# Kernel optimization log

Hardware: AMD Instinct MI355X
Metric: run time of the kernel (lower is better)

## Reference

```python
import jax, jax.numpy as jnp
import numpy as np

N_NODES = 100000
N_EDGES = 800000
IN_DIM = 128
NUM_HEADS = 8
HEAD_DIM = 16  # out_dim // num_heads = 128 // 8


def setup_inputs() -> dict:
    key = jax.random.key(0)
    ks = jax.random.split(key, 10)
    scale = 1.0 / np.sqrt(IN_DIM)
    return {
        "x": jax.random.normal(ks[0], (N_NODES, IN_DIM), dtype=jnp.float32),
        "edge_index": jax.random.randint(ks[1], (2, N_EDGES), 0, N_NODES, dtype=jnp.int64),
        "virt_h": jax.random.normal(ks[2], (1, IN_DIM), dtype=jnp.float32),
        "virt_edge_index": jax.random.randint(ks[3], (2, 1), 0, 1, dtype=jnp.int64),
        "Wq": jax.random.normal(ks[4], (IN_DIM, NUM_HEADS * HEAD_DIM), dtype=jnp.float32) * scale,
        "bq": jnp.zeros((NUM_HEADS * HEAD_DIM,), dtype=jnp.float32),
        "Wk": jax.random.normal(ks[5], (IN_DIM, NUM_HEADS * HEAD_DIM), dtype=jnp.float32) * scale,
        "bk": jnp.zeros((NUM_HEADS * HEAD_DIM,), dtype=jnp.float32),
        "Wv": jax.random.normal(ks[6], (IN_DIM, NUM_HEADS * HEAD_DIM), dtype=jnp.float32) * scale,
        "bv": jnp.zeros((NUM_HEADS * HEAD_DIM,), dtype=jnp.float32),
    }


def reference(x, edge_index, virt_h, virt_edge_index, Wq, bq, Wk, bk, Wv, bv):
    # use_virt_nodes=False: virt_h / virt_edge_index are unused dummies.
    n = x.shape[0]
    H, D = NUM_HEADS, HEAD_DIM
    Q = (x @ Wq + bq).reshape(n, H, D)
    K = (x @ Wk + bk).reshape(n, H, D)
    V = (x @ Wv + bv).reshape(n, H, D)

    src = edge_index[0]
    dst = edge_index[1]

    # edge-wise gather QK dot -> clamp -> exp; score: [E, H, 1]
    dot = jnp.sum(K[src] * Q[dst], axis=-1, keepdims=True) / np.sqrt(D).astype(np.float32)
    score = jnp.exp(jnp.clip(dot, -5.0, 5.0))

    msg = V[src] * score  # [E, H, D]
    wV = jax.ops.segment_sum(msg, dst, num_segments=n)     # [N, H, D]
    Z = jax.ops.segment_sum(score, dst, num_segments=n)    # [N, H, 1]

    h_out = (wV / (Z + 1e-6)).reshape(n, H * D)
    return h_out
```

## Files before the change

### kernel.cpp

```cpp
#include <hip/hip_runtime.h>

#define IN_DIM   128
#define NH       8
#define HD       16
#define OUTD     128
#define QKVD     384
#define SH       7
#define NSORTB   128
#define GRID     1024

typedef unsigned short ushort_t;
typedef unsigned int   uint_t;
typedef __bf16 bf16x8 __attribute__((ext_vector_type(8)));
typedef float  f32x4  __attribute__((ext_vector_type(4)));

__device__ __forceinline__ float bf2f(ushort_t u) {
    return __uint_as_float(((uint_t)u) << 16);
}
__device__ __forceinline__ ushort_t f2bf(float f) {
    uint_t u = __float_as_uint(f);
    u += 0x7FFFu + ((u >> 16) & 1u);
    return (ushort_t)(u >> 16);
}

__global__ __launch_bounds__(256) void prep_w(
    const float* __restrict__ Wq, const float* __restrict__ Wk,
    const float* __restrict__ Wv, ushort_t* __restrict__ Wt)
{
    __shared__ float ld[32][33];
    int mat  = blockIdx.x >> 4;
    int tile = blockIdx.x & 15;
    int k0 = (tile >> 2) * 32, c0 = (tile & 3) * 32;
    const float* W = (mat == 0) ? Wq : (mat == 1) ? Wk : Wv;
    int t = threadIdx.x;
    {
        int k = t >> 3, c4 = (t & 7) * 4;
        float4 f = *(const float4*)&W[(size_t)(k0 + k) * 128 + c0 + c4];
        ld[k][c4 + 0] = f.x; ld[k][c4 + 1] = f.y;
        ld[k][c4 + 2] = f.z; ld[k][c4 + 3] = f.w;
    }
    __syncthreads();
    {
        int c = t >> 3, kg = (t & 7) * 4;
        union { ushort_t h[4]; uint2 u; } o;
        o.h[0] = f2bf(ld[kg + 0][c]); o.h[1] = f2bf(ld[kg + 1][c]);
        o.h[2] = f2bf(ld[kg + 2][c]); o.h[3] = f2bf(ld[kg + 3][c]);
        *(uint2*)&Wt[((size_t)(mat * 128 + c0 + c)) * 128 + k0 + kg] = o.u;
    }
}

__global__ __launch_bounds__(384, 3) void fat_gemm_sort(
    const float* __restrict__ x, const ushort_t* __restrict__ Wt,
    const float* __restrict__ bq, const float* __restrict__ bk,
    const float* __restrict__ bv, ushort_t* __restrict__ qkv,
    const int* __restrict__ ei, int* __restrict__ aux,
    uint_t* __restrict__ regions,
    int N, int E, int ntiles, int NBC, int CH)
{
    __shared__ __align__(16) char smem[33192];

    if (blockIdx.x < NSORTB) {
        uint_t* recs = (uint_t*)smem;
        int* hist    = (int*)(smem + 25000);
        int* scn     = (int*)(smem + 29096);
        const int tid = threadIdx.x;
        const int blk = blockIdx.x;
        const int e0g = blk * CH;
        const int e1g = min(E, e0g + CH);
        const int m   = e1g - e0g;

        for (int i = tid; i < 1024; i += 384) hist[i] = 0;
        __syncthreads();
        for (int e = e0g + tid; e < e1g; e += 384)
            atomicAdd(&hist[ei[E + e] >> SH], 1);
        __syncthreads();
        if (tid < 64) {
            int base16 = tid * 16;
            int loc[16]; int s = 0;
#pragma unroll
            for (int i = 0; i < 16; i++) { loc[i] = s; s += hist[base16 + i]; }
            int incl = s;
            for (int off = 1; off < 64; off <<= 1) {
                int t = __shfl_up(incl, off);
                if (tid >= off) incl += t;
            }
            int cexcl = incl - s;
#pragma unroll
            for (int i = 0; i < 16; i++) scn[base16 + i] = cexcl + loc[i];
        }
        __syncthreads();
        for (int b = tid; b < NBC; b += 384) aux[b * NSORTB + blk] = scn[b];
        if (tid == 0) aux[NBC * NSORTB + blk] = m;
        __syncthreads();
        for (int e = e0g + tid; e < e1g; e += 384) {
            int d = ei[E + e];
            int src = ei[e];
            int slot = atomicAdd(&scn[d >> SH], 1);
            recs[slot] = (uint_t)src | ((uint_t)(d & 127) << 20);
        }
        __syncthreads();
        for (int s = tid; s < m; s += 384)
            regions[(size_t)blk * CH + s] = recs[s];
        return;
    }

    ushort_t* sh = (ushort_t*)smem;

    const int tid  = threadIdx.x;
    const int w    = tid >> 6;
    const int quad = (tid >> 4) & 3;
    const int l15  = tid & 15;
    const int colg = w << 6;

    bf16x8 bfr[4][4];
#pragma unroll
    for (int kt = 0; kt < 4; kt++)
#pragma unroll
        for (int cs = 0; cs < 4; cs++) {
            int col = colg + cs * 16 + l15;
            bfr[kt][cs] = *(const bf16x8*)&Wt[(size_t)col * 128 + kt * 32 + quad * 8];
        }

    const int mat = w >> 1;
    const float* Bp = (mat == 0) ? bq : (mat == 1) ? bk : bv;
    float bias[4];
#pragma unroll
    for (int cs = 0; cs < 4; cs++)
        bias[cs] = Bp[((w & 1) << 6) + cs * 16 + l15];

    const int gstride = (int)gridDim.x - NSORTB;
    for (int tile = (int)blockIdx.x - NSORTB; tile < ntiles; tile += gstride) {
        const int row0 = tile * 64;
        __syncthreads();

        for (int ch = tid; ch < 1024; ch += 384) {
            int row = ch >> 4;
            int kc  = ch & 15;
            int grow = row0 + row; if (grow > N - 1) grow = N - 1;
            const float* xp = x + (size_t)grow * IN_DIM + kc * 8;
            float4 f0 = *(const float4*)xp;
            float4 f1 = *(const float4*)(xp + 4);
            union { ushort_t h[8]; uint4 u; } tt;
            tt.h[0] = f2bf(f0.x); tt.h[1] = f2bf(f0.y);
            tt.h[2] = f2bf(f0.z); tt.h[3] = f2bf(f0.w);
            tt.h[4] = f2bf(f1.x); tt.h[5] = f2bf(f1.y);
            tt.h[6] = f2bf(f1.z); tt.h[7] = f2bf(f1.w);
            *(uint4*)&sh[(kc * 65 + row) * 8] = tt.u;
        }
        __syncthreads();

        f32x4 acc[4][4];
#pragma unroll
        for (int r = 0; r < 4; r++)
#pragma unroll
            for (int cs = 0; cs < 4; cs++) acc[r][cs] = (f32x4){0.f, 0.f, 0.f, 0.f};

#pragma unroll
        for (int kt = 0; kt < 4; kt++) {
            int kc = kt * 4 + quad;
            bf16x8 af[4];
#pragma unroll
            for (int r = 0; r < 4; r++)
                af[r] = *(const bf16x8*)&sh[(kc * 65 + r * 16 + l15) * 8];
#pragma unroll
            for (int r = 0; r < 4; r++)
#pragma unroll
                for (int cs = 0; cs < 4; cs++)
                    acc[r][cs] = __builtin_amdgcn_mfma_f32_16x16x32_bf16(
                        af[r], bfr[kt][cs], acc[r][cs], 0, 0, 0);
        }

#define EPS 392
#pragma unroll
        for (int qq = 0; qq < 4; qq++) {
            __syncthreads();
            int lrow = quad << 2;
#pragma unroll
            for (int cs = 0; cs < 4; cs++) {
                int col = (w << 6) + cs * 16 + l15;
#pragma unroll
                for (int reg = 0; reg < 4; reg++)
                    sh[(lrow + reg) * EPS + col] = f2bf(acc[qq][cs][reg] + bias[cs]);
            }
            __syncthreads();
#pragma unroll
            for (int i = 0; i < 2; i++) {
                int c = tid + i * 384;
                int row = c / 48;
                int col = (c % 48) * 8;
                int grow = row0 + qq * 16 + row;
                if (grow < N) {
                    uint4 val = *(const uint4*)&sh[row * EPS + col];
                    *(uint4*)&qkv[(size_t)grow * QKVD + col] = val;
                }
            }
        }
#undef EPS
    }
}

__global__ __launch_bounds__(256) void efine(
    const uint_t* __restrict__ regions, const int* __restrict__ aux,
    int* __restrict__ P, int* __restrict__ sorted_src,
    int N, int NBC, int CH)
{
    __shared__ int rl[128], ro[128], doff[128];
    __shared__ int cnt[128], scn2[128];
    __shared__ uint_t stage[4096];
    __shared__ int    sst[4096];
    __shared__ int s_part[2];
    const int tid = threadIdx.x;
    const int b   = blockIdx.x;

    if (tid < 128) {
        int r0 = aux[b * NSORTB + tid];
        int r1 = aux[(b + 1) * NSORTB + tid];
        ro[tid] = r0;
        rl[tid] = r1 - r0;
        doff[tid] = r1 - r0;
        int bsum = r0;
#pragma unroll
        for (int off = 1; off < 64; off <<= 1)
            bsum += __shfl_xor(bsum, off);
        if ((tid & 63) == 0) s_part[tid >> 6] = bsum;
    }
    __syncthreads();
    for (int off = 1; off < 128; off <<= 1) {
        int v = (tid >= off && tid < 128) ? doff[tid - off] : 0;
        __syncthreads();
        if (tid < 128) doff[tid] += v;
        __syncthreads();
    }
    const int m = doff[127];
    const int base = s_part[0] + s_part[1];

    {
        int r = tid >> 1, k = tid & 1;
        int dst0 = doff[r] - rl[r];
        int src0 = ro[r];
        int len  = rl[r];
        for (int i = k; i < len; i += 2)
            stage[dst0 + i] = regions[(size_t)r * CH + src0 + i];
    }
    __syncthreads();

    if (tid < 128) cnt[tid] = 0;
    __syncthreads();
    for (int i = tid; i < m; i += 256)
        atomicAdd(&cnt[stage[i] >> 20], 1);
    __syncthreads();
    if (tid < 128) scn2[tid] = cnt[tid];
    __syncthreads();
    for (int off = 1; off < 128; off <<= 1) {
        int v = (tid >= off && tid < 128) ? scn2[tid - off] : 0;
        __syncthreads();
        if (tid < 128) scn2[tid] += v;
        __syncthreads();
    }
    if (tid < 128) {
        int excl = scn2[tid] - cnt[tid];
        int n = b * 128 + tid;
        if (n < N) P[n] = base + excl;
        cnt[tid] = excl;
    }
    __syncthreads();
    for (int i = tid; i < m; i += 256) {
        uint_t r = stage[i];
        int pos = atomicAdd(&cnt[r >> 20], 1);
        sst[pos] = (int)(r & 0xFFFFFu);
    }
    __syncthreads();
    for (int i = tid; i < m; i += 256)
        sorted_src[base + i] = sst[i];
}

__global__ __launch_bounds__(256) void segment_attn(
    const ushort_t* __restrict__ qkv,
    const int* __restrict__ P, const int* __restrict__ sorted_src,
    float* __restrict__ out, int N, int E)
{
    int n = (blockIdx.x * 256 + threadIdx.x) >> 4;
    int g = threadIdx.x & 15;
    if (n >= N) return;
    int start = P[n];
    int end   = (n + 1 < N) ? P[n + 1] : E;
    int deg   = end - start;

    const uint_t* qrow = (const uint_t*)(qkv + (size_t)n * QKVD);
    uint4 qu = *(const uint4*)(qrow + g * 4);
    float q0 = bf2f((ushort_t)(qu.x & 0xFFFF)), q1 = bf2f((ushort_t)(qu.x >> 16));
    float q2 = bf2f((ushort_t)(qu.y & 0xFFFF)), q3 = bf2f((ushort_t)(qu.y >> 16));
    float q4 = bf2f((ushort_t)(qu.z & 0xFFFF)), q5 = bf2f((ushort_t)(qu.z >> 16));
    float q6 = bf2f((ushort_t)(qu.w & 0xFFFF)), q7 = bf2f((ushort_t)(qu.w >> 16));

    float a0 = 0.f, a1 = 0.f, a2 = 0.f, a3 = 0.f;
    float a4 = 0.f, a5 = 0.f, a6 = 0.f, a7 = 0.f, z = 0.f;

    int myidx = (g < deg) ? sorted_src[start + g] : 0;
    int wbase = (threadIdx.x & 63) & 48;

#define PROC(ku, vu)                                                       \
    {                                                                      \
        float p = bf2f((ushort_t)((ku).x & 0xFFFF)) * q0                   \
                + bf2f((ushort_t)((ku).x >> 16))    * q1                   \
                + bf2f((ushort_t)((ku).y & 0xFFFF)) * q2                   \
                + bf2f((ushort_t)((ku).y >> 16))    * q3                   \
                + bf2f((ushort_t)((ku).z & 0xFFFF)) * q4                   \
                + bf2f((ushort_t)((ku).z >> 16))    * q5                   \
                + bf2f((ushort_t)((ku).w & 0xFFFF)) * q6                   \
                + bf2f((ushort_t)((ku).w >> 16))    * q7;                  \
        p += __shfl_xor(p, 1);                                             \
        p = fminf(fmaxf(p * 0.25f, -5.f), 5.f);                            \
        float s = __expf(p);                                               \
        a0 += bf2f((ushort_t)((vu).x & 0xFFFF)) * s;                       \
        a1 += bf2f((ushort_t)((vu).x >> 16))    * s;                       \
        a2 += bf2f((ushort_t)((vu).y & 0xFFFF)) * s;                       \
        a3 += bf2f((ushort_t)((vu).y >> 16))    * s;                       \
        a4 += bf2f((ushort_t)((vu).z & 0xFFFF)) * s;                       \
        a5 += bf2f((ushort_t)((vu).z >> 16))    * s;                       \
        a6 += bf2f((ushort_t)((vu).w & 0xFFFF)) * s;                       \
        a7 += bf2f((ushort_t)((vu).w >> 16))    * s;                       \
        z += s;                                                            \
    }

    int cnt = (deg < 16) ? deg : 16;
    int t = 0;
    for (; t + 4 <= cnt; t += 4) {
        int s0 = __shfl(myidx, wbase + t);
        int s1 = __shfl(myidx, wbase + t + 1);
        int s2 = __shfl(myidx, wbase + t + 2);
        int s3 = __shfl(myidx, wbase + t + 3);
        const uint_t* kv0 = (const uint_t*)(qkv + (size_t)s0 * QKVD + 128);
        const uint_t* kv1 = (const uint_t*)(qkv + (size_t)s1 * QKVD + 128);
        const uint_t* kv2 = (const uint_t*)(qkv + (size_t)s2 * QKVD + 128);
        const uint_t* kv3 = (const uint_t*)(qkv + (size_t)s3 * QKVD + 128);
        uint4 ku0 = *(const uint4*)(kv0 + g * 4);
        uint4 ku1 = *(const uint4*)(kv1 + g * 4);
        uint4 ku2 = *(const uint4*)(kv2 + g * 4);
        uint4 ku3 = *(const uint4*)(kv3 + g * 4);
        uint4 vu0 = *(const uint4*)(kv0 + 64 + g * 4);
        uint4 vu1 = *(const uint4*)(kv1 + 64 + g * 4);
        uint4 vu2 = *(const uint4*)(kv2 + 64 + g * 4);
        uint4 vu3 = *(const uint4*)(kv3 + 64 + g * 4);
        PROC(ku0, vu0); PROC(ku1, vu1); PROC(ku2, vu2); PROC(ku3, vu3);
    }
    for (; t + 2 <= cnt; t += 2) {
        int s0 = __shfl(myidx, wbase + t);
        int s1 = __shfl(myidx, wbase + t + 1);
        const uint_t* kv0 = (const uint_t*)(qkv + (size_t)s0 * QKVD + 128);
        const uint_t* kv1 = (const uint_t*)(qkv + (size_t)s1 * QKVD + 128);
        uint4 ku0 = *(const uint4*)(kv0 + g * 4);
        uint4 ku1 = *(const uint4*)(kv1 + g * 4);
        uint4 vu0 = *(const uint4*)(kv0 + 64 + g * 4);
        uint4 vu1 = *(const uint4*)(kv1 + 64 + g * 4);
        PROC(ku0, vu0); PROC(ku1, vu1);
    }
    if (t < cnt) {
        int s0 = __shfl(myidx, wbase + t);
        const uint_t* kv0 = (const uint_t*)(qkv + (size_t)s0 * QKVD + 128);
        uint4 ku0 = *(const uint4*)(kv0 + g * 4);
        uint4 vu0 = *(const uint4*)(kv0 + 64 + g * 4);
        PROC(ku0, vu0);
    }
    for (int j = start + 16; j + 2 <= end; j += 2) {
        int s0 = sorted_src[j];
        int s1 = sorted_src[j + 1];
        const uint_t* kv0 = (const uint_t*)(qkv + (size_t)s0 * QKVD + 128);
        const uint_t* kv1 = (const uint_t*)(qkv + (size_t)s1 * QKVD + 128);
        uint4 ku0 = *(const uint4*)(kv0 + g * 4);
        uint4 ku1 = *(const uint4*)(kv1 + g * 4);
        uint4 vu0 = *(const uint4*)(kv0 + 64 + g * 4);
        uint4 vu1 = *(const uint4*)(kv1 + 64 + g * 4);
        PROC(ku0, vu0); PROC(ku1, vu1);
    }
    if (deg > 16 && ((deg - 16) & 1)) {
        int s0 = sorted_src[end - 1];
        const uint_t* kv0 = (const uint_t*)(qkv + (size_t)s0 * QKVD + 128);
        uint4 ku0 = *(const uint4*)(kv0 + g * 4);
        uint4 vu0 = *(const uint4*)(kv0 + 64 + g * 4);
        PROC(ku0, vu0);
    }
#undef PROC

    float inv = 1.f / (z + 1e-6f);
    f32x4 o0 = {a0 * inv, a1 * inv, a2 * inv, a3 * inv};
    f32x4 o1 = {a4 * inv, a5 * inv, a6 * inv, a7 * inv};
    float* ob = out + (size_t)n * OUTD + g * 8;
    __builtin_nontemporal_store(o0, (f32x4*)ob);
    __builtin_nontemporal_store(o1, (f32x4*)(ob + 4));
}

extern "C" void kernel_launch(void* const* d_in, const int* in_sizes, int n_in,
                              void* d_out, int out_size, void* d_ws, size_t ws_size,
                              hipStream_t stream) {
    const float* x  = (const float*)d_in[0];
    const int*   ei = (const int*)d_in[1];
    const float* Wq = (const float*)d_in[4];
    const float* bq = (const float*)d_in[5];
    const float* Wk = (const float*)d_in[6];
    const float* bk = (const float*)d_in[7];
    const float* Wv = (const float*)d_in[8];
    const float* bv = (const float*)d_in[9];
    float* out = (float*)d_out;

    const int N = in_sizes[0] / IN_DIM;
    const int E = in_sizes[1] / 2;
    const int NBC = (N + 127) >> 7;
    const int CH  = (E + NSORTB - 1) / NSORTB;

    char* wsb = (char*)d_ws;
    ushort_t* qkv = (ushort_t*)wsb;
    ushort_t* Wt  = qkv + (size_t)N * QKVD;
    int* aux = (int*)(Wt + 384 * 128);
    uint_t* regions = (uint_t*)(aux + (NBC + 1) * NSORTB);
    int* sorted = (int*)(regions + (size_t)NSORTB * CH);
    int* P = sorted + E;

    const int ntiles = (N + 63) / 64;

    prep_w<<<48, 256, 0, stream>>>(Wq, Wk, Wv, Wt);
    fat_gemm_sort<<<GRID, 384, 0, stream>>>(
        x, Wt, bq, bk, bv, qkv, ei, aux, regions, N, E, ntiles, NBC, CH);
    efine<<<NBC, 256, 0, stream>>>(regions, aux, P, sorted, N, NBC, CH);
    segment_attn<<<((size_t)N * 16 + 255) / 256, 256, 0, stream>>>(
        qkv, P, sorted, out, N, E);
}
```

Baseline: 240.5 us.

## Fuse weight prep and fine sort into GEMM kernel with grid barrier

Drops the separate weight-transpose kernel; each GEMM wave now reads fp32 weights directly with strided loads and converts them to bf16 in registers. The efine bucket-sort pass moves into the sort blocks of the fat kernel: after a spin-wait barrier across the 128 sort blocks, they pull bucket work from an atomic counter. This removes two launches and their gaps, and lets the fine sort overlap the GEMM tail. In exchange it adds a memset, a spin barrier that assumes all 128 sort blocks are co-resident, and uncoalesced weight loads per GEMM block.

```diff
diff --git a/kernel.cpp b/kernel.cpp
--- a/kernel.cpp
+++ b/kernel.cpp
@@ -14,6 +14,8 @@
 typedef __bf16 bf16x8 __attribute__((ext_vector_type(8)));
 typedef float  f32x4  __attribute__((ext_vector_type(4)));
 
+#define AGT __HIP_MEMORY_SCOPE_AGENT
+
 __device__ __forceinline__ float bf2f(ushort_t u) {
     return __uint_as_float(((uint_t)u) << 16);
 }
@@ -23,106 +25,175 @@
     return (ushort_t)(u >> 16);
 }
 
-__global__ __launch_bounds__(256) void prep_w(
-    const float* __restrict__ Wq, const float* __restrict__ Wk,
-    const float* __restrict__ Wv, ushort_t* __restrict__ Wt)
-{
-    __shared__ float ld[32][33];
-    int mat  = blockIdx.x >> 4;
-    int tile = blockIdx.x & 15;
-    int k0 = (tile >> 2) * 32, c0 = (tile & 3) * 32;
-    const float* W = (mat == 0) ? Wq : (mat == 1) ? Wk : Wv;
-    int t = threadIdx.x;
-    {
-        int k = t >> 3, c4 = (t & 7) * 4;
-        float4 f = *(const float4*)&W[(size_t)(k0 + k) * 128 + c0 + c4];
-        ld[k][c4 + 0] = f.x; ld[k][c4 + 1] = f.y;
-        ld[k][c4 + 2] = f.z; ld[k][c4 + 3] = f.w;
-    }
-    __syncthreads();
-    {
-        int c = t >> 3, kg = (t & 7) * 4;
-        union { ushort_t h[4]; uint2 u; } o;
-        o.h[0] = f2bf(ld[kg + 0][c]); o.h[1] = f2bf(ld[kg + 1][c]);
-        o.h[2] = f2bf(ld[kg + 2][c]); o.h[3] = f2bf(ld[kg + 3][c]);
-        *(uint2*)&Wt[((size_t)(mat * 128 + c0 + c)) * 128 + k0 + kg] = o.u;
-    }
-}
-
-__global__ __launch_bounds__(384, 3) void fat_gemm_sort(
-    const float* __restrict__ x, const ushort_t* __restrict__ Wt,
-    const float* __restrict__ bq, const float* __restrict__ bk,
-    const float* __restrict__ bv, ushort_t* __restrict__ qkv,
+__global__ __launch_bounds__(384, 3) void fat_all(
+    const float* __restrict__ x,
+    const float* __restrict__ Wq, const float* __restrict__ bq,
+    const float* __restrict__ Wk, const float* __restrict__ bk,
+    const float* __restrict__ Wv, const float* __restrict__ bv,
+    ushort_t* __restrict__ qkv,
     const int* __restrict__ ei, int* __restrict__ aux,
     uint_t* __restrict__ regions,
+    int* __restrict__ P, int* __restrict__ sorted_src, int* ctr,
     int N, int E, int ntiles, int NBC, int CH)
 {
-    __shared__ __align__(16) char smem[33192];
+    __shared__ __align__(16) char smem[35344];
+    const int tid = threadIdx.x;
 
     if (blockIdx.x < NSORTB) {
-        uint_t* recs = (uint_t*)smem;
-        int* hist    = (int*)(smem + 25000);
-        int* scn     = (int*)(smem + 29096);
-        const int tid = threadIdx.x;
-        const int blk = blockIdx.x;
-        const int e0g = blk * CH;
-        const int e1g = min(E, e0g + CH);
-        const int m   = e1g - e0g;
-
-        for (int i = tid; i < 1024; i += 384) hist[i] = 0;
+        {
+            uint_t* recs = (uint_t*)smem;
+            int* hist    = (int*)(smem + 25000);
+            int* scn     = (int*)(smem + 29096);
+            const int blk = blockIdx.x;
+            const int e0g = blk * CH;
+            const int e1g = min(E, e0g + CH);
+            const int m   = e1g - e0g;
+
+            for (int i = tid; i < 1024; i += 384) hist[i] = 0;
+            __syncthreads();
+            for (int e = e0g + tid; e < e1g; e += 384)
+                atomicAdd(&hist[ei[E + e] >> SH], 1);
+            __syncthreads();
+            if (tid < 64) {
+                int base16 = tid * 16;
+                int loc[16]; int s = 0;
+#pragma unroll
+                for (int i = 0; i < 16; i++) { loc[i] = s; s += hist[base16 + i]; }
+                int incl = s;
+                for (int off = 1; off < 64; off <<= 1) {
+                    int t = __shfl_up(incl, off);
+                    if (tid >= off) incl += t;
+                }
+                int cexcl = incl - s;
+#pragma unroll
+                for (int i = 0; i < 16; i++) scn[base16 + i] = cexcl + loc[i];
+            }
+            __syncthreads();
+            for (int b = tid; b < NBC; b += 384) aux[b * NSORTB + blk] = scn[b];
+            if (tid == 0) aux[NBC * NSORTB + blk] = m;
+            __syncthreads();
+            for (int e = e0g + tid; e < e1g; e += 384) {
+                int d = ei[E + e];
+                int src = ei[e];
+                int slot = atomicAdd(&scn[d >> SH], 1);
+                recs[slot] = (uint_t)src | ((uint_t)(d & 127) << 20);
+            }
+            __syncthreads();
+            for (int s = tid; s < m; s += 384)
+                regions[(size_t)blk * CH + s] = recs[s];
+        }
         __syncthreads();
-        for (int e = e0g + tid; e < e1g; e += 384)
-            atomicAdd(&hist[ei[E + e] >> SH], 1);
+        if (tid == 0) {
+            __hip_atomic_fetch_add(&ctr[0], 1, __ATOMIC_RELEASE, AGT);
+            while (__hip_atomic_load(&ctr[0], __ATOMIC_RELAXED, AGT) < NSORTB)
+                __builtin_amdgcn_s_sleep(8);
+            (void)__hip_atomic_load(&ctr[0], __ATOMIC_ACQUIRE, AGT);
+        }
         __syncthreads();
-        if (tid < 64) {
-            int base16 = tid * 16;
-            int loc[16]; int s = 0;
-#pragma unroll
-            for (int i = 0; i < 16; i++) { loc[i] = s; s += hist[base16 + i]; }
-            int incl = s;
-            for (int off = 1; off < 64; off <<= 1) {
-                int t = __shfl_up(incl, off);
-                if (tid >= off) incl += t;
-            }
-            int cexcl = incl - s;
-#pragma unroll
-            for (int i = 0; i < 16; i++) scn[base16 + i] = cexcl + loc[i];
-        }
-        __syncthreads();
-        for (int b = tid; b < NBC; b += 384) aux[b * NSORTB + blk] = scn[b];
-        if (tid == 0) aux[NBC * NSORTB + blk] = m;
-        __syncthreads();
-        for (int e = e0g + tid; e < e1g; e += 384) {
-            int d = ei[E + e];
-            int src = ei[e];
-            int slot = atomicAdd(&scn[d >> SH], 1);
-            recs[slot] = (uint_t)src | ((uint_t)(d & 127) << 20);
-        }
-        __syncthreads();
-        for (int s = tid; s < m; s += 384)
-            regions[(size_t)blk * CH + s] = recs[s];
+
+        uint_t* stage = (uint_t*)smem;
+        int* sst   = (int*)(smem + 16384);
+        int* rl    = (int*)(smem + 32768);
+        int* ro    = (int*)(smem + 33280);
+        int* doff  = (int*)(smem + 33792);
+        int* cnt   = (int*)(smem + 34304);
+        int* scn2  = (int*)(smem + 34816);
+        int* sparts = (int*)(smem + 35328);
+        int* s_word = (int*)(smem + 35336);
+
+        for (;;) {
+            __syncthreads();
+            if (tid == 0)
+                *s_word = __hip_atomic_fetch_add(&ctr[1], 1, __ATOMIC_RELAXED, AGT);
+            __syncthreads();
+            const int b = *s_word;
+            if (b >= NBC) break;
+
+            if (tid < 128) {
+                int r0 = aux[b * NSORTB + tid];
+                int r1 = aux[(b + 1) * NSORTB + tid];
+                ro[tid] = r0; rl[tid] = r1 - r0; doff[tid] = r1 - r0;
+                int bsum = r0;
+#pragma unroll
+                for (int off = 1; off < 64; off <<= 1)
+                    bsum += __shfl_xor(bsum, off);
+                if ((tid & 63) == 0) sparts[tid >> 6] = bsum;
+            }
+            __syncthreads();
+            for (int off = 1; off < 128; off <<= 1) {
+                int v = (tid >= off && tid < 128) ? doff[tid - off] : 0;
+                __syncthreads();
+                if (tid < 128) doff[tid] += v;
+                __syncthreads();
+            }
+            const int m2  = doff[127];
+            const int base = sparts[0] + sparts[1];
+
+            {
+                int r = tid >> 1, k = tid & 1;
+                if (r < 128) {
+                    int dst0 = doff[r] - rl[r];
+                    int src0 = ro[r];
+                    int len  = rl[r];
+                    for (int i = k; i < len; i += 2)
+                        stage[dst0 + i] = regions[(size_t)r * CH + src0 + i];
+                }
+            }
+            __syncthreads();
+
+            if (tid < 128) cnt[tid] = 0;
+            __syncthreads();
+            for (int i = tid; i < m2; i += 384)
+                atomicAdd(&cnt[stage[i] >> 20], 1);
+            __syncthreads();
+            if (tid < 128) scn2[tid] = cnt[tid];
+            __syncthreads();
+            for (int off = 1; off < 128; off <<= 1) {
+                int v = (tid >= off && tid < 128) ? scn2[tid - off] : 0;
+                __syncthreads();
+                if (tid < 128) scn2[tid] += v;
+                __syncthreads();
+            }
+            if (tid < 128) {
+                int excl = scn2[tid] - cnt[tid];
+                int n = b * 128 + tid;
+                if (n < N) P[n] = base + excl;
+                cnt[tid] = excl;
+            }
+            __syncthreads();
+            for (int i = tid; i < m2; i += 384) {
+                uint_t r = stage[i];
+                int pos = atomicAdd(&cnt[r >> 20], 1);
+                sst[pos] = (int)(r & 0xFFFFFu);
+            }
+            __syncthreads();
+            for (int i = tid; i < m2; i += 384)
+                sorted_src[base + i] = sst[i];
+        }
         return;
     }
 
     ushort_t* sh = (ushort_t*)smem;
 
-    const int tid  = threadIdx.x;
     const int w    = tid >> 6;
     const int quad = (tid >> 4) & 3;
     const int l15  = tid & 15;
-    const int colg = w << 6;
+    const int mat  = w >> 1;
+    const float* Wsel = (mat == 0) ? Wq : (mat == 1) ? Wk : Wv;
+    const float* Bp   = (mat == 0) ? bq : (mat == 1) ? bk : bv;
 
     bf16x8 bfr[4][4];
 #pragma unroll
     for (int kt = 0; kt < 4; kt++)
 #pragma unroll
         for (int cs = 0; cs < 4; cs++) {
-            int col = colg + cs * 16 + l15;
-            bfr[kt][cs] = *(const bf16x8*)&Wt[(size_t)col * 128 + kt * 32 + quad * 8];
-        }
-
-    const int mat = w >> 1;
-    const float* Bp = (mat == 0) ? bq : (mat == 1) ? bk : bv;
+            int c = ((w & 1) << 6) + cs * 16 + l15;
+            union { ushort_t h[8]; bf16x8 v; } u;
+#pragma unroll
+            for (int j = 0; j < 8; j++)
+                u.h[j] = f2bf(Wsel[(size_t)(kt * 32 + quad * 8 + j) * 128 + c]);
+            bfr[kt][cs] = u.v;
+        }
     float bias[4];
 #pragma unroll
     for (int cs = 0; cs < 4; cs++)
@@ -197,81 +268,6 @@
         }
 #undef EPS
     }
-}
-
-__global__ __launch_bounds__(256) void efine(
-    const uint_t* __restrict__ regions, const int* __restrict__ aux,
-    int* __restrict__ P, int* __restrict__ sorted_src,
-    int N, int NBC, int CH)
-{
-    __shared__ int rl[128], ro[128], doff[128];
-    __shared__ int cnt[128], scn2[128];
-    __shared__ uint_t stage[4096];
-    __shared__ int    sst[4096];
-    __shared__ int s_part[2];
-    const int tid = threadIdx.x;
-    const int b   = blockIdx.x;
-
-    if (tid < 128) {
-        int r0 = aux[b * NSORTB + tid];
-        int r1 = aux[(b + 1) * NSORTB + tid];
-        ro[tid] = r0;
-        rl[tid] = r1 - r0;
-        doff[tid] = r1 - r0;
-        int bsum = r0;
-#pragma unroll
-        for (int off = 1; off < 64; off <<= 1)
-            bsum += __shfl_xor(bsum, off);
-        if ((tid & 63) == 0) s_part[tid >> 6] = bsum;
-    }
-    __syncthreads();
-    for (int off = 1; off < 128; off <<= 1) {
-        int v = (tid >= off && tid < 128) ? doff[tid - off] : 0;
-        __syncthreads();
-        if (tid < 128) doff[tid] += v;
-        __syncthreads();
-    }
-    const int m = doff[127];
-    const int base = s_part[0] + s_part[1];
-
-    {
-        int r = tid >> 1, k = tid & 1;
-        int dst0 = doff[r] - rl[r];
-        int src0 = ro[r];
-        int len  = rl[r];
-        for (int i = k; i < len; i += 2)
-            stage[dst0 + i] = regions[(size_t)r * CH + src0 + i];
-    }
-    __syncthreads();
-
-    if (tid < 128) cnt[tid] = 0;
-    __syncthreads();
-    for (int i = tid; i < m; i += 256)
-        atomicAdd(&cnt[stage[i] >> 20], 1);
-    __syncthreads();
-    if (tid < 128) scn2[tid] = cnt[tid];
-    __syncthreads();
-    for (int off = 1; off < 128; off <<= 1) {
-        int v = (tid >= off && tid < 128) ? scn2[tid - off] : 0;
-        __syncthreads();
-        if (tid < 128) scn2[tid] += v;
-        __syncthreads();
-    }
-    if (tid < 128) {
-        int excl = scn2[tid] - cnt[tid];
-        int n = b * 128 + tid;
-        if (n < N) P[n] = base + excl;
-        cnt[tid] = excl;
-    }
-    __syncthreads();
-    for (int i = tid; i < m; i += 256) {
-        uint_t r = stage[i];
-        int pos = atomicAdd(&cnt[r >> 20], 1);
-        sst[pos] = (int)(r & 0xFFFFFu);
-    }
-    __syncthreads();
-    for (int i = tid; i < m; i += 256)
-        sorted_src[base + i] = sst[i];
 }
 
 __global__ __launch_bounds__(256) void segment_attn(
@@ -410,18 +406,18 @@
 
     char* wsb = (char*)d_ws;
     ushort_t* qkv = (ushort_t*)wsb;
-    ushort_t* Wt  = qkv + (size_t)N * QKVD;
-    int* aux = (int*)(Wt + 384 * 128);
+    int* aux = (int*)(qkv + (size_t)N * QKVD);
     uint_t* regions = (uint_t*)(aux + (NBC + 1) * NSORTB);
     int* sorted = (int*)(regions + (size_t)NSORTB * CH);
     int* P = sorted + E;
+    int* ctr = P + N;
 
     const int ntiles = (N + 63) / 64;
 
-    prep_w<<<48, 256, 0, stream>>>(Wq, Wk, Wv, Wt);
-    fat_gemm_sort<<<GRID, 384, 0, stream>>>(
-        x, Wt, bq, bk, bv, qkv, ei, aux, regions, N, E, ntiles, NBC, CH);
-    efine<<<NBC, 256, 0, stream>>>(regions, aux, P, sorted, N, NBC, CH);
+    hipMemsetAsync(ctr, 0, 8, stream);
+    fat_all<<<GRID, 384, 0, stream>>>(
+        x, Wq, bq, Wk, bk, Wv, bv, qkv, ei, aux, regions,
+        P, sorted, ctr, N, E, ntiles, NBC, CH);
     segment_attn<<<((size_t)N * 16 + 255) / 256, 256, 0, stream>>>(
         qkv, P, sorted, out, N, E);
 }
```

Measured after the change: 261.3 us. 8.6% more time.
